# Performance work log

Hardware: AMD Instinct MI355X
Metric: run time of the kernel (lower is better)

Reference implementation:

```python
import jax, jax.numpy as jnp
import numpy as np

B, P, G, C = 16, 32768, 32, 81   # batch, priors, gt boxes per image, classes
IOU_THRESH = 0.5                 # matching() is IoU-threshold matching (standard SSD)
HMR = 3                          # hard_mining_ratio
BETA = 1.0                       # SmoothL1 beta


def _make_boxes(key, lead_shape):
    k1, k2 = jax.random.split(key)
    xy = jax.random.uniform(k1, lead_shape + (2,)) * 0.8
    wh = jax.random.uniform(k2, lead_shape + (2,)) * 0.2 + 0.05
    return jnp.concatenate([xy, xy + wh], axis=-1)  # valid x1y1x2y2 in [0,1]


def setup_inputs() -> dict:
    key = jax.random.key(0)
    ks = jax.random.split(key, 5)
    pred_boxes = _make_boxes(ks[0], (B, P))
    gt_boxes = _make_boxes(ks[1], (B, G))
    # guarantee matches exist: first G priors track the gt boxes closely
    noise = jax.random.normal(ks[2], (B, G, 4)) * 0.005
    pred_boxes = pred_boxes.at[:, :G, :].set(gt_boxes + noise)
    pred_confidences = jax.random.normal(ks[3], (B, P, C), dtype=jnp.float32)
    gt_labels = jax.random.randint(ks[4], (B, G), 0, C, dtype=jnp.int32)
    return {"pred_boxes": pred_boxes, "pred_confidences": pred_confidences,
            "gt_boxes": gt_boxes, "gt_labels": gt_labels}


def _iou(a, b):
    # a: [P,4], b: [G,4] in x1y1x2y2 -> [P,G]
    lt = jnp.maximum(a[:, None, :2], b[None, :, :2])
    rb = jnp.minimum(a[:, None, 2:], b[None, :, 2:])
    inter = jnp.prod(jnp.clip(rb - lt, 0.0), axis=-1)
    area_a = jnp.prod(jnp.clip(a[:, 2:] - a[:, :2], 0.0), axis=-1)
    area_b = jnp.prod(jnp.clip(b[:, 2:] - b[:, :2], 0.0), axis=-1)
    union = area_a[:, None] + area_b[None, :] - inter
    return inter / jnp.maximum(union, 1e-9)


def _smooth_l1(pred, gt):
    d = pred - gt
    ad = jnp.abs(d)
    return jnp.where(ad < BETA, 0.5 * d * d / BETA, ad - 0.5 * BETA)


def _per_image(boxes, conf, gboxes, glabels):
    # boxes [P,4], conf [P,C], gboxes [G,4], glabels [G]
    matches = _iou(boxes, gboxes) > IOU_THRESH          # [P,G]
    total = matches.sum()
    logsm = jax.nn.log_softmax(conf, axis=-1)            # [P,C]
    gathered = logsm[:, glabels]                         # [P,G] log p(label_g | prior_i)
    matches_loss = jnp.sum(jnp.where(matches, gathered, 0.0))
    # mean over the 4 coords, summed over matched (prior, gt) pairs
    sl1 = _smooth_l1(boxes[:, None, :], gboxes[None, :, :]).mean(axis=-1)  # [P,G]
    loc_loss = jnp.sum(jnp.where(matches, sl1, 0.0))
    # hard-negative mining over unmatched priors
    row_matched = matches.any(axis=1)                    # [P]
    sm_max = jnp.max(jax.nn.softmax(conf, axis=-1), axis=-1)  # [P], all > 0
    neg = jnp.where(row_matched, -1.0, sm_max)           # matched rows sort last
    neg = jnp.concatenate([neg, jnp.zeros((1,), neg.dtype)])  # source's extra slot (contributes log1p(0)=0)
    sorted_neg = -jnp.sort(-neg)                         # descending
    k = HMR * total
    keep = (jnp.arange(sorted_neg.shape[0]) < k) & (sorted_neg >= 0.0)
    nomatch_loss = jnp.sum(jnp.where(keep, jnp.log1p(sorted_neg), 0.0))
    return matches_loss, nomatch_loss, loc_loss, total


def reference(pred_boxes, pred_confidences, gt_boxes, gt_labels):
    m, n, l, t = jax.vmap(_per_image)(pred_boxes, pred_confidences, gt_boxes, gt_labels)
    conf_loss = -m.sum() + n.sum()
    # faithful to source: final division uses the LAST image's total_matches
    total_last = t[-1].astype(conf_loss.dtype)
    return (conf_loss + l.sum()) / total_last
```

## Files before the change

### kernel.cpp

```cpp
#include <hip/hip_runtime.h>
#include <hip/hip_bf16.h>
#include <math.h>

#define BB 16
#define PP 32768
#define GG 32
#define NC 81
#define BINSHIFT 13
#define NBINS 8192
#define LOWMASK 0x1FFFu
#define BINBASE 0x3B800000u
#define CAND_CAP 2048
#define SENT 0x7FFFFFFFu
#define SM_BLOCKS 2048
#define BLK_PER_IMG 128
#define NEGINF (-3.0e38f)

struct Accs {
  float m[BB]; float l[BB]; float n[BB];
  unsigned tot[BB]; unsigned rowm[BB];
  unsigned tbin[BB]; unsigned rem[BB]; unsigned candcnt[BB];
};

__device__ __forceinline__ int bin_of(unsigned bits) {
  int bin = ((int)bits - (int)BINBASE) >> BINSHIFT;
  return bin < 0 ? 0 : (bin > NBINS - 1 ? NBINS - 1 : bin);
}

__global__ void init_kernel(Accs* __restrict__ acc) {
  const int t = threadIdx.x;
  if (t < BB) {
    acc->m[t] = 0.f; acc->l[t] = 0.f; acc->n[t] = 0.f;
    acc->tot[t] = 0u; acc->rowm[t] = 0u; acc->candcnt[t] = 0u;
  }
}

__global__ __launch_bounds__(256) void main_kernel(
    const float* __restrict__ pred_boxes,
    const float* __restrict__ conf,
    const float* __restrict__ gt_boxes,
    const int*   __restrict__ gt_labels,
    float* __restrict__ neg,
    Accs* __restrict__ acc)
{
  const int tid  = threadIdx.x;
  const int j    = tid & 7;
  const int rsub = tid >> 3;
  const int b    = blockIdx.x / BLK_PER_IMG;
  const int loc  = blockIdx.x % BLK_PER_IMG;
  const int lane = tid & 63;
  const int w    = tid >> 6;

  __shared__ unsigned s_gm[NC + 3];
  __shared__ float pg[4], pl[4];
  __shared__ unsigned pc[4], pr[4];

  if (tid < NC + 3) s_gm[tid] = 0u;
  __syncthreads();
  if (tid < GG) atomicOr(&s_gm[gt_labels[b * GG + tid]], 1u << tid);
  __syncthreads();

  const float4* gtb = ((const float4*)gt_boxes) + b * GG;
  const float4 gA = gtb[j];
  const float4 gB = gtb[j + 8];
  const float4 gC = gtb[j + 16];
  const float4 gD = gtb[j + 24];
  const float abA = fmaxf(gA.z - gA.x, 0.f) * fmaxf(gA.w - gA.y, 0.f);
  const float abB = fmaxf(gB.z - gB.x, 0.f) * fmaxf(gB.w - gB.y, 0.f);
  const float abC = fmaxf(gC.z - gC.x, 0.f) * fmaxf(gC.w - gC.y, 0.f);
  const float abD = fmaxf(gD.z - gD.x, 0.f) * fmaxf(gD.w - gD.y, 0.f);

  const int  h  = rsub & 3;
  const bool j0 = (j == 0), j4 = (j == 4);
  const bool has3 = (j < 5);
  const float mA0 = (j0 && h > 0) ? NEGINF : 0.f;
  const float mA1 = (j0 && h > 1) ? NEGINF : 0.f;
  const float mA2 = (j0 && h > 2) ? NEGINF : 0.f;
  const float mC1 = (j4 && h < 1) ? NEGINF : 0.f;
  const float mC2 = (j4 && h < 2) ? NEGINF : 0.f;
  const float mC3 = (j4 && h < 3) ? NEGINF : 0.f;
  const int dA = 4 * j - h;
  const int dB = 4 * (j + 8) - h;
  const int dC = 4 * (j + 16) - h;

  const float4* cf = (const float4*)conf;
  const float4* pbf = (const float4*)pred_boxes;

  float t_g = 0.f, t_l = 0.f;
  unsigned t_c = 0u, t_r = 0u;

  int row = b * PP + loc * 32 + rsub;
  {
    const unsigned abase = (81u * (unsigned)row) >> 2;
  }
  unsigned abase0 = (81u * (unsigned)row) >> 2;
  float4 va = cf[abase0 + j];
  float4 vb = cf[abase0 + j + 8];
  float4 vc = has3 ? cf[abase0 + j + 16] : va;
  float4 pb = pbf[row];

  #pragma unroll
  for (int k = 0; k < 8; ++k) {
    float4 nva = va, nvb = vb, nvc = vc, npb = pb;
    if (k < 7) {
      const int nrow = row + BLK_PER_IMG * 32;
      const unsigned nab = (81u * (unsigned)nrow) >> 2;
      nva = cf[nab + j];
      nvb = cf[nab + j + 8];
      if (has3) nvc = cf[nab + j + 16]; else nvc = nva;
      npb = pbf[nrow];
    }

    const float a0 = va.x + mA0, a1 = va.y + mA1, a2 = va.z + mA2, a3 = va.w;
    float mx = fmaxf(fmaxf(a0, a1), fmaxf(a2, a3));
    float s  = __expf(a0) + __expf(a1) + __expf(a2) + __expf(a3);
    mx = fmaxf(mx, fmaxf(fmaxf(vb.x, vb.y), fmaxf(vb.z, vb.w)));
    s += __expf(vb.x) + __expf(vb.y) + __expf(vb.z) + __expf(vb.w);
    if (has3) {
      const float e0 = vc.x, e1 = vc.y + mC1, e2 = vc.z + mC2, e3 = vc.w + mC3;
      mx = fmaxf(mx, fmaxf(fmaxf(e0, e1), fmaxf(e2, e3)));
      s += __expf(e0) + __expf(e1) + __expf(e2) + __expf(e3);
    }
    mx = fmaxf(mx, __shfl_xor(mx, 1));  s += __shfl_xor(s, 1);
    mx = fmaxf(mx, __shfl_xor(mx, 2));  s += __shfl_xor(s, 2);
    mx = fmaxf(mx, __shfl_xor(mx, 4));  s += __shfl_xor(s, 4);
    const float lse = __logf(s);
    const float smx = __expf(mx - lse);

    const float aa = fmaxf(pb.z - pb.x, 0.f) * fmaxf(pb.w - pb.y, 0.f);
    unsigned msk = 0u;
    unsigned mymt = 0u;
    #define IOU_ONE(gb, ab, sh, bit)                                        \
    {                                                                       \
      const float ltx = fmaxf(pb.x, gb.x), lty = fmaxf(pb.y, gb.y);         \
      const float rbx = fminf(pb.z, gb.z), rby = fminf(pb.w, gb.w);         \
      const float inter = fmaxf(rbx - ltx, 0.f) * fmaxf(rby - lty, 0.f);    \
      const float uni = aa + ab - inter;                                    \
      const bool mt = inter > 0.5f * fmaxf(uni, 1e-9f);                     \
      msk  |= mt ? (1u << (j + sh)) : 0u;                                   \
      mymt |= mt ? (1u << bit) : 0u;                                        \
    }
    IOU_ONE(gA, abA, 0, 0)
    IOU_ONE(gB, abB, 8, 1)
    IOU_ONE(gC, abC, 16, 2)
    IOU_ONE(gD, abD, 24, 3)
    #undef IOU_ONE

    msk |= __shfl_xor(msk, 1); msk |= __shfl_xor(msk, 2); msk |= __shfl_xor(msk, 4);

    if (j == 0) neg[row] = (msk != 0u) ? -1.0f : smx;

    if (__any(msk != 0u)) {
      float lsum = 0.f;
      #define SL1_ONE(gb, bit)                                              \
      if (mymt & (1u << bit)) {                                             \
        const float d0 = pb.x - gb.x, d1 = pb.y - gb.y;                     \
        const float d2 = pb.z - gb.z, d3 = pb.w - gb.w;                     \
        float sl = 0.f, ad;                                                 \
        ad = fabsf(d0); sl += (ad < 1.f) ? 0.5f * d0 * d0 : ad - 0.5f;      \
        ad = fabsf(d1); sl += (ad < 1.f) ? 0.5f * d1 * d1 : ad - 0.5f;      \
        ad = fabsf(d2); sl += (ad < 1.f) ? 0.5f * d2 * d2 : ad - 0.5f;      \
        ad = fabsf(d3); sl += (ad < 1.f) ? 0.5f * d3 * d3 : ad - 0.5f;      \
        lsum += sl * 0.25f;                                                 \
      }
      SL1_ONE(gA, 0)
      SL1_ONE(gB, 1)
      SL1_ONE(gC, 2)
      SL1_ONE(gD, 3)
      #undef SL1_ONE
      t_l += lsum;

      if (msk != 0u) {
        float gsum = 0.f;
        if (dA >= 0) gsum += va.x * (float)__popc(msk & s_gm[dA]);
        if (dA + 1 >= 0) gsum += va.y * (float)__popc(msk & s_gm[dA + 1]);
        if (dA + 2 >= 0) gsum += va.z * (float)__popc(msk & s_gm[dA + 2]);
        gsum += va.w * (float)__popc(msk & s_gm[dA + 3]);
        gsum += vb.x * (float)__popc(msk & s_gm[dB]);
        gsum += vb.y * (float)__popc(msk & s_gm[dB + 1]);
        gsum += vb.z * (float)__popc(msk & s_gm[dB + 2]);
        gsum += vb.w * (float)__popc(msk & s_gm[dB + 3]);
        if (has3) {
          gsum += vc.x * (float)__popc(msk & s_gm[dC]);
          if (dC + 1 < NC) gsum += vc.y * (float)__popc(msk & s_gm[dC + 1]);
          if (dC + 2 < NC) gsum += vc.z * (float)__popc(msk & s_gm[dC + 2]);
          if (dC + 3 < NC) gsum += vc.w * (float)__popc(msk & s_gm[dC + 3]);
        }
        t_g += gsum;
        if (j == 0) {
          const unsigned cnt = (unsigned)__popc(msk);
          t_g -= (float)cnt * lse;
          t_c += cnt;
          t_r += 1u;
        }
      }
    }

    va = nva; vb = nvb; vc = nvc; pb = npb;
    row += BLK_PER_IMG * 32;
  }

  t_g += __shfl_xor(t_g, 1);  t_l += __shfl_xor(t_l, 1);  t_c += __shfl_xor(t_c, 1);  t_r += __shfl_xor(t_r, 1);
  t_g += __shfl_xor(t_g, 2);  t_l += __shfl_xor(t_l, 2);  t_c += __shfl_xor(t_c, 2);  t_r += __shfl_xor(t_r, 2);
  t_g += __shfl_xor(t_g, 4);  t_l += __shfl_xor(t_l, 4);  t_c += __shfl_xor(t_c, 4);  t_r += __shfl_xor(t_r, 4);
  t_g += __shfl_xor(t_g, 8);  t_l += __shfl_xor(t_l, 8);  t_c += __shfl_xor(t_c, 8);  t_r += __shfl_xor(t_r, 8);
  t_g += __shfl_xor(t_g, 16); t_l += __shfl_xor(t_l, 16); t_c += __shfl_xor(t_c, 16); t_r += __shfl_xor(t_r, 16);
  t_g += __shfl_xor(t_g, 32); t_l += __shfl_xor(t_l, 32); t_c += __shfl_xor(t_c, 32); t_r += __shfl_xor(t_r, 32);
  if (lane == 0) { pg[w] = t_g; pl[w] = t_l; pc[w] = t_c; pr[w] = t_r; }
  __syncthreads();
  if (tid == 0) {
    const unsigned c2 = pc[0] + pc[1] + pc[2] + pc[3];
    if (c2 > 0u) {
      atomicAdd(&acc->m[b],    pg[0] + pg[1] + pg[2] + pg[3]);
      atomicAdd(&acc->l[b],    pl[0] + pl[1] + pl[2] + pl[3]);
      atomicAdd(&acc->tot[b],  c2);
      atomicAdd(&acc->rowm[b], pr[0] + pr[1] + pr[2] + pr[3]);
    }
  }
}

__global__ __launch_bounds__(256) void thresh_kernel(const float* __restrict__ neg,
                                                     Accs* __restrict__ acc) {
  const int b = blockIdx.x, tid = threadIdx.x;
  __shared__ unsigned hist[NBINS];
  __shared__ unsigned ps[256];
  __shared__ unsigned s_ch, s_cb;

  const unsigned total  = acc->tot[b];
  const unsigned nvalid = PP - acc->rowm[b];
  unsigned K = 3u * total;
  if (K > nvalid) K = nvalid;
  if (K == 0u) {
    if (tid == 0) { acc->tbin[b] = SENT; acc->rem[b] = 0u; }
    return;
  }

  for (int i = tid; i < NBINS; i += 256) hist[i] = 0u;
  __syncthreads();

  const float4* nb = (const float4*)(neg + ((size_t)b << 15));
  for (int i = tid; i < PP / 4; i += 256) {
    const float4 v4 = nb[i];
    const float vv[4] = {v4.x, v4.y, v4.z, v4.w};
    #pragma unroll
    for (int q = 0; q < 4; ++q)
      if (vv[q] >= 0.f) atomicAdd(&hist[bin_of(__float_as_uint(vv[q]))], 1u);
  }
  __syncthreads();

  unsigned loc = 0;
  #pragma unroll
  for (int q = 0; q < NBINS / 256; ++q) loc += hist[tid * (NBINS / 256) + q];
  ps[tid] = loc;
  __syncthreads();
  for (int off = 1; off < 256; off <<= 1) {
    const unsigned v = (tid + off < 256) ? ps[tid + off] : 0u;
    __syncthreads();
    ps[tid] += v;
    __syncthreads();
  }
  {
    const unsigned above = (tid < 255) ? ps[tid + 1] : 0u;
    if (ps[tid] >= K && above < K) { s_ch = (unsigned)tid; s_cb = above; }
  }
  __syncthreads();
  const unsigned ch = s_ch, cb = s_cb;
  const int CH = NBINS / 256;
  if (tid < CH) ps[tid] = hist[ch * CH + tid];
  __syncthreads();
  for (int off = 1; off < CH; off <<= 1) {
    const unsigned v = (tid < CH && tid + off < CH) ? ps[tid + off] : 0u;
    __syncthreads();
    if (tid < CH) ps[tid] += v;
    __syncthreads();
  }
  if (tid < CH) {
    const unsigned above = cb + ((tid < CH - 1) ? ps[tid + 1] : 0u);
    if (above < K && cb + ps[tid] >= K) {
      acc->tbin[b] = ch * (unsigned)CH + (unsigned)tid;
      acc->rem[b]  = K - above;
    }
  }
}

__global__ __launch_bounds__(256) void sum_kernel(const float* __restrict__ neg,
                                                  float* __restrict__ cand,
                                                  Accs* __restrict__ acc) {
  const int b  = blockIdx.x >> 4;
  const int sl = blockIdx.x & 15;
  const unsigned t = acc->tbin[b];
  const float4* nb = (const float4*)(neg + ((size_t)b << 15)) + sl * 512;
  float sum = 0.f;
  #pragma unroll
  for (int it = 0; it < 2; ++it) {
    const float4 v4 = nb[threadIdx.x + it * 256];
    const float vv[4] = {v4.x, v4.y, v4.z, v4.w};
    #pragma unroll
    for (int q = 0; q < 4; ++q) {
      const float v = vv[q];
      if (v >= 0.f) {
        const unsigned bin = (unsigned)bin_of(__float_as_uint(v));
        if (bin > t) {
          sum += log1pf(v);
        } else if (bin == t) {
          const unsigned idx = atomicAdd(&acc->candcnt[b], 1u);
          if (idx < CAND_CAP) cand[(size_t)b * CAND_CAP + idx] = v;
        }
      }
    }
  }
  sum += __shfl_xor(sum, 1);  sum += __shfl_xor(sum, 2);  sum += __shfl_xor(sum, 4);
  sum += __shfl_xor(sum, 8);  sum += __shfl_xor(sum, 16); sum += __shfl_xor(sum, 32);
  if ((threadIdx.x & 63) == 0 && sum != 0.f) atomicAdd(&acc->n[b], sum);
}

__global__ __launch_bounds__(256) void refine_kernel(const float* __restrict__ neg,
                                                     const float* __restrict__ cand,
                                                     Accs* __restrict__ acc) {
  const int b = blockIdx.x, tid = threadIdx.x;
  __shared__ unsigned h2[NBINS];
  __shared__ unsigned ps[256];
  __shared__ unsigned s_thr, s_rem2;
  const unsigned t = acc->tbin[b];
  if (t == SENT) return;
  const unsigned rem = acc->rem[b];
  const unsigned cc  = acc->candcnt[b];
  const bool fb = (cc > CAND_CAP);
  const int n_src = fb ? PP : (int)cc;
  const float* src = fb ? (neg + ((size_t)b << 15)) : (cand + (size_t)b * CAND_CAP);

  for (int i = tid; i < NBINS; i += 256) h2[i] = 0u;
  __syncthreads();
  for (int i = tid; i < n_src; i += 256) {
    const float v = src[i];
    if (fb) {
      if (!(v >= 0.f) || (unsigned)bin_of(__float_as_uint(v)) != t) continue;
    }
    atomicAdd(&h2[__float_as_uint(v) & LOWMASK], 1u);
  }
  __syncthreads();

  unsigned loc = 0;
  #pragma unroll
  for (int q = 0; q < NBINS / 256; ++q) loc += h2[tid * (NBINS / 256) + q];
  ps[tid] = loc;
  __syncthreads();
  for (int off = 1; off < 256; off <<= 1) {
    const unsigned v = (tid + off < 256) ? ps[tid + off] : 0u;
    __syncthreads();
    ps[tid] += v;
    __syncthreads();
  }
  {
    const unsigned above = (tid < 255) ? ps[tid + 1] : 0u;
    if (ps[tid] >= rem && above < rem) {
      unsigned c = above;
      const int CH = NBINS / 256;
      for (int q = CH - 1; q >= 0; --q) {
        const unsigned hb = h2[tid * CH + q];
        if (c + hb >= rem) { s_thr = (unsigned)(tid * CH + q); s_rem2 = rem - c; break; }
        c += hb;
      }
    }
  }
  __syncthreads();
  const unsigned thr = s_thr, rem2 = s_rem2;

  float sum = 0.f;
  for (int i = tid; i < n_src; i += 256) {
    const float v = src[i];
    if (fb) {
      if (!(v >= 0.f) || (unsigned)bin_of(__float_as_uint(v)) != t) continue;
    }
    if ((__float_as_uint(v) & LOWMASK) > thr) sum += log1pf(v);
  }
  sum += __shfl_xor(sum, 1);  sum += __shfl_xor(sum, 2);  sum += __shfl_xor(sum, 4);
  sum += __shfl_xor(sum, 8);  sum += __shfl_xor(sum, 16); sum += __shfl_xor(sum, 32);
  if ((tid & 63) == 0 && sum != 0.f) atomicAdd(&acc->n[b], sum);
  if (tid == 0 && rem2 > 0u) {
    const unsigned tb = BINBASE + (t << BINSHIFT) + thr;
    atomicAdd(&acc->n[b], (float)rem2 * log1pf(__uint_as_float(tb)));
  }
}

__global__ void finish_kernel(const Accs* __restrict__ acc, float* __restrict__ out) {
  if (threadIdx.x == 0) {
    float conf = 0.f, loc = 0.f;
    #pragma unroll
    for (int b = 0; b < BB; ++b) {
      conf += -acc->m[b] + acc->n[b];
      loc  += acc->l[b];
    }
    out[0] = (conf + loc) / (float)acc->tot[BB - 1];
  }
}

extern "C" void kernel_launch(void* const* d_in, const int* in_sizes, int n_in,
                              void* d_out, int out_size, void* d_ws, size_t ws_size,
                              hipStream_t stream) {
  const float* pred_boxes = (const float*)d_in[0];
  const float* conf       = (const float*)d_in[1];
  const float* gt_boxes   = (const float*)d_in[2];
  const int*   gt_labels  = (const int*)d_in[3];
  float* out = (float*)d_out;

  char* ws = (char*)d_ws;
  float* neg  = (float*)ws;
  float* cand = (float*)(ws + (size_t)BB * PP * 4);
  Accs*  acc  = (Accs*)(ws + (size_t)BB * PP * 4 + (size_t)BB * CAND_CAP * 4);

  hipLaunchKernelGGL(init_kernel, dim3(1), dim3(64), 0, stream, acc);
  hipLaunchKernelGGL(main_kernel, dim3(SM_BLOCKS), dim3(256), 0, stream,
                     pred_boxes, conf, gt_boxes, gt_labels, neg, acc);
  hipLaunchKernelGGL(thresh_kernel, dim3(BB), dim3(256), 0, stream, neg, acc);
  hipLaunchKernelGGL(sum_kernel, dim3(BB * 16), dim3(256), 0, stream, neg, cand, acc);
  hipLaunchKernelGGL(refine_kernel, dim3(BB), dim3(256), 0, stream, neg, cand, acc);
  hipLaunchKernelGGL(finish_kernel, dim3(1), dim3(64), 0, stream, acc, out);
}
```

Before: 104.5 us.

## Fuse threshold, sum and refine kernels into single per-image select kernel

```diff
diff --git a/kernel.cpp b/kernel.cpp
--- a/kernel.cpp
+++ b/kernel.cpp
@@ -10,8 +10,6 @@
 #define NBINS 8192
 #define LOWMASK 0x1FFFu
 #define BINBASE 0x3B800000u
-#define CAND_CAP 2048
-#define SENT 0x7FFFFFFFu
 #define SM_BLOCKS 2048
 #define BLK_PER_IMG 128
 #define NEGINF (-3.0e38f)
@@ -19,7 +17,6 @@
 struct Accs {
   float m[BB]; float l[BB]; float n[BB];
   unsigned tot[BB]; unsigned rowm[BB];
-  unsigned tbin[BB]; unsigned rem[BB]; unsigned candcnt[BB];
 };
 
 __device__ __forceinline__ int bin_of(unsigned bits) {
@@ -31,7 +28,7 @@
   const int t = threadIdx.x;
   if (t < BB) {
     acc->m[t] = 0.f; acc->l[t] = 0.f; acc->n[t] = 0.f;
-    acc->tot[t] = 0u; acc->rowm[t] = 0u; acc->candcnt[t] = 0u;
+    acc->tot[t] = 0u; acc->rowm[t] = 0u;
   }
 }
 
@@ -83,20 +80,17 @@
   const int dB = 4 * (j + 8) - h;
   const int dC = 4 * (j + 16) - h;
 
-  const float4* cf = (const float4*)conf;
+  const float4* cf  = (const float4*)conf;
   const float4* pbf = (const float4*)pred_boxes;
 
   float t_g = 0.f, t_l = 0.f;
   unsigned t_c = 0u, t_r = 0u;
 
   int row = b * PP + loc * 32 + rsub;
-  {
-    const unsigned abase = (81u * (unsigned)row) >> 2;
-  }
-  unsigned abase0 = (81u * (unsigned)row) >> 2;
-  float4 va = cf[abase0 + j];
-  float4 vb = cf[abase0 + j + 8];
-  float4 vc = has3 ? cf[abase0 + j + 16] : va;
+  const unsigned ab0 = (81u * (unsigned)row) >> 2;
+  float4 va = cf[ab0 + j];
+  float4 vb = cf[ab0 + j + 8];
+  float4 vc = has3 ? cf[ab0 + j + 16] : va;
   float4 pb = pbf[row];
 
   #pragma unroll
@@ -219,23 +213,26 @@
   }
 }
 
-__global__ __launch_bounds__(256) void thresh_kernel(const float* __restrict__ neg,
-                                                     Accs* __restrict__ acc) {
+__global__ __launch_bounds__(256) void select_kernel(const float* __restrict__ neg,
+                                                     Accs* __restrict__ acc)
+{
   const int b = blockIdx.x, tid = threadIdx.x;
   __shared__ unsigned hist[NBINS];
+  __shared__ unsigned h2[NBINS];
   __shared__ unsigned ps[256];
-  __shared__ unsigned s_ch, s_cb;
+  __shared__ unsigned s_ch, s_cb, s_t, s_remv, s_thr, s_rem2;
+  __shared__ float spart[4];
 
   const unsigned total  = acc->tot[b];
   const unsigned nvalid = PP - acc->rowm[b];
   unsigned K = 3u * total;
   if (K > nvalid) K = nvalid;
   if (K == 0u) {
-    if (tid == 0) { acc->tbin[b] = SENT; acc->rem[b] = 0u; }
+    if (tid == 0) acc->n[b] = 0.f;
     return;
   }
 
-  for (int i = tid; i < NBINS; i += 256) hist[i] = 0u;
+  for (int i = tid; i < NBINS; i += 256) { hist[i] = 0u; h2[i] = 0u; }
   __syncthreads();
 
   const float4* nb = (const float4*)(neg + ((size_t)b << 15));
@@ -248,139 +245,97 @@
   }
   __syncthreads();
 
-  unsigned loc = 0;
-  #pragma unroll
-  for (int q = 0; q < NBINS / 256; ++q) loc += hist[tid * (NBINS / 256) + q];
-  ps[tid] = loc;
-  __syncthreads();
-  for (int off = 1; off < 256; off <<= 1) {
-    const unsigned v = (tid + off < 256) ? ps[tid + off] : 0u;
-    __syncthreads();
-    ps[tid] += v;
-    __syncthreads();
-  }
   {
+    unsigned loc = 0;
+    #pragma unroll
+    for (int q = 0; q < 32; ++q) loc += hist[tid * 32 + q];
+    ps[tid] = loc;
+    __syncthreads();
+    for (int off = 1; off < 256; off <<= 1) {
+      const unsigned v = (tid + off < 256) ? ps[tid + off] : 0u;
+      __syncthreads();
+      ps[tid] += v;
+      __syncthreads();
+    }
     const unsigned above = (tid < 255) ? ps[tid + 1] : 0u;
     if (ps[tid] >= K && above < K) { s_ch = (unsigned)tid; s_cb = above; }
-  }
-  __syncthreads();
-  const unsigned ch = s_ch, cb = s_cb;
-  const int CH = NBINS / 256;
-  if (tid < CH) ps[tid] = hist[ch * CH + tid];
-  __syncthreads();
-  for (int off = 1; off < CH; off <<= 1) {
-    const unsigned v = (tid < CH && tid + off < CH) ? ps[tid + off] : 0u;
-    __syncthreads();
-    if (tid < CH) ps[tid] += v;
-    __syncthreads();
-  }
-  if (tid < CH) {
-    const unsigned above = cb + ((tid < CH - 1) ? ps[tid + 1] : 0u);
-    if (above < K && cb + ps[tid] >= K) {
-      acc->tbin[b] = ch * (unsigned)CH + (unsigned)tid;
-      acc->rem[b]  = K - above;
-    }
-  }
-}
-
-__global__ __launch_bounds__(256) void sum_kernel(const float* __restrict__ neg,
-                                                  float* __restrict__ cand,
-                                                  Accs* __restrict__ acc) {
-  const int b  = blockIdx.x >> 4;
-  const int sl = blockIdx.x & 15;
-  const unsigned t = acc->tbin[b];
-  const float4* nb = (const float4*)(neg + ((size_t)b << 15)) + sl * 512;
+    __syncthreads();
+    const unsigned ch = s_ch, cb = s_cb;
+    if (tid < 32) ps[tid] = hist[ch * 32 + tid];
+    __syncthreads();
+    for (int off = 1; off < 32; off <<= 1) {
+      const unsigned v = (tid < 32 && tid + off < 32) ? ps[tid + off] : 0u;
+      __syncthreads();
+      if (tid < 32) ps[tid] += v;
+      __syncthreads();
+    }
+    if (tid < 32) {
+      const unsigned ab2 = cb + ((tid < 31) ? ps[tid + 1] : 0u);
+      if (ab2 < K && cb + ps[tid] >= K) { s_t = ch * 32u + (unsigned)tid; s_remv = K - ab2; }
+    }
+    __syncthreads();
+  }
+  const unsigned t   = s_t;
+  const unsigned rem = s_remv;
+
   float sum = 0.f;
-  #pragma unroll
-  for (int it = 0; it < 2; ++it) {
-    const float4 v4 = nb[threadIdx.x + it * 256];
+  for (int i = tid; i < PP / 4; i += 256) {
+    const float4 v4 = nb[i];
     const float vv[4] = {v4.x, v4.y, v4.z, v4.w};
     #pragma unroll
     for (int q = 0; q < 4; ++q) {
       const float v = vv[q];
       if (v >= 0.f) {
-        const unsigned bin = (unsigned)bin_of(__float_as_uint(v));
-        if (bin > t) {
-          sum += log1pf(v);
-        } else if (bin == t) {
-          const unsigned idx = atomicAdd(&acc->candcnt[b], 1u);
-          if (idx < CAND_CAP) cand[(size_t)b * CAND_CAP + idx] = v;
-        }
+        const unsigned bits = __float_as_uint(v);
+        const unsigned bin = (unsigned)bin_of(bits);
+        if (bin > t) sum += log1pf(v);
+        else if (bin == t) atomicAdd(&h2[bits & LOWMASK], 1u);
       }
     }
   }
-  sum += __shfl_xor(sum, 1);  sum += __shfl_xor(sum, 2);  sum += __shfl_xor(sum, 4);
-  sum += __shfl_xor(sum, 8);  sum += __shfl_xor(sum, 16); sum += __shfl_xor(sum, 32);
-  if ((threadIdx.x & 63) == 0 && sum != 0.f) atomicAdd(&acc->n[b], sum);
-}
-
-__global__ __launch_bounds__(256) void refine_kernel(const float* __restrict__ neg,
-                                                     const float* __restrict__ cand,
-                                                     Accs* __restrict__ acc) {
-  const int b = blockIdx.x, tid = threadIdx.x;
-  __shared__ unsigned h2[NBINS];
-  __shared__ unsigned ps[256];
-  __shared__ unsigned s_thr, s_rem2;
-  const unsigned t = acc->tbin[b];
-  if (t == SENT) return;
-  const unsigned rem = acc->rem[b];
-  const unsigned cc  = acc->candcnt[b];
-  const bool fb = (cc > CAND_CAP);
-  const int n_src = fb ? PP : (int)cc;
-  const float* src = fb ? (neg + ((size_t)b << 15)) : (cand + (size_t)b * CAND_CAP);
-
-  for (int i = tid; i < NBINS; i += 256) h2[i] = 0u;
-  __syncthreads();
-  for (int i = tid; i < n_src; i += 256) {
-    const float v = src[i];
-    if (fb) {
-      if (!(v >= 0.f) || (unsigned)bin_of(__float_as_uint(v)) != t) continue;
-    }
-    atomicAdd(&h2[__float_as_uint(v) & LOWMASK], 1u);
-  }
-  __syncthreads();
-
-  unsigned loc = 0;
-  #pragma unroll
-  for (int q = 0; q < NBINS / 256; ++q) loc += h2[tid * (NBINS / 256) + q];
-  ps[tid] = loc;
-  __syncthreads();
-  for (int off = 1; off < 256; off <<= 1) {
-    const unsigned v = (tid + off < 256) ? ps[tid + off] : 0u;
-    __syncthreads();
-    ps[tid] += v;
-    __syncthreads();
-  }
+  __syncthreads();
+
   {
+    unsigned loc = 0;
+    #pragma unroll
+    for (int q = 0; q < 32; ++q) loc += h2[tid * 32 + q];
+    ps[tid] = loc;
+    __syncthreads();
+    for (int off = 1; off < 256; off <<= 1) {
+      const unsigned v = (tid + off < 256) ? ps[tid + off] : 0u;
+      __syncthreads();
+      ps[tid] += v;
+      __syncthreads();
+    }
     const unsigned above = (tid < 255) ? ps[tid + 1] : 0u;
     if (ps[tid] >= rem && above < rem) {
       unsigned c = above;
-      const int CH = NBINS / 256;
-      for (int q = CH - 1; q >= 0; --q) {
-        const unsigned hb = h2[tid * CH + q];
-        if (c + hb >= rem) { s_thr = (unsigned)(tid * CH + q); s_rem2 = rem - c; break; }
+      for (int q = 31; q >= 0; --q) {
+        const unsigned hb = h2[tid * 32 + q];
+        if (c + hb >= rem) { s_thr = (unsigned)(tid * 32 + q); s_rem2 = rem - c; break; }
         c += hb;
       }
     }
-  }
-  __syncthreads();
+    __syncthreads();
+  }
   const unsigned thr = s_thr, rem2 = s_rem2;
 
-  float sum = 0.f;
-  for (int i = tid; i < n_src; i += 256) {
-    const float v = src[i];
-    if (fb) {
-      if (!(v >= 0.f) || (unsigned)bin_of(__float_as_uint(v)) != t) continue;
-    }
-    if ((__float_as_uint(v) & LOWMASK) > thr) sum += log1pf(v);
-  }
+  const unsigned base_t = BINBASE + (t << BINSHIFT);
+  #pragma unroll
+  for (int q = 0; q < 32; ++q) {
+    const unsigned low = (unsigned)tid * 32u + (unsigned)q;
+    const unsigned c = h2[low];
+    if (low > thr && c > 0u)
+      sum += (float)c * log1pf(__uint_as_float(base_t + low));
+  }
+  if (tid == 0)
+    sum += (float)rem2 * log1pf(__uint_as_float(base_t + thr));
+
   sum += __shfl_xor(sum, 1);  sum += __shfl_xor(sum, 2);  sum += __shfl_xor(sum, 4);
   sum += __shfl_xor(sum, 8);  sum += __shfl_xor(sum, 16); sum += __shfl_xor(sum, 32);
-  if ((tid & 63) == 0 && sum != 0.f) atomicAdd(&acc->n[b], sum);
-  if (tid == 0 && rem2 > 0u) {
-    const unsigned tb = BINBASE + (t << BINSHIFT) + thr;
-    atomicAdd(&acc->n[b], (float)rem2 * log1pf(__uint_as_float(tb)));
-  }
+  if ((tid & 63) == 0) spart[tid >> 6] = sum;
+  __syncthreads();
+  if (tid == 0) acc->n[b] = spart[0] + spart[1] + spart[2] + spart[3];
 }
 
 __global__ void finish_kernel(const Accs* __restrict__ acc, float* __restrict__ out) {
@@ -405,15 +360,12 @@
   float* out = (float*)d_out;
 
   char* ws = (char*)d_ws;
-  float* neg  = (float*)ws;
-  float* cand = (float*)(ws + (size_t)BB * PP * 4);
-  Accs*  acc  = (Accs*)(ws + (size_t)BB * PP * 4 + (size_t)BB * CAND_CAP * 4);
+  float* neg = (float*)ws;
+  Accs*  acc = (Accs*)(ws + (size_t)BB * PP * 4);
 
   hipLaunchKernelGGL(init_kernel, dim3(1), dim3(64), 0, stream, acc);
   hipLaunchKernelGGL(main_kernel, dim3(SM_BLOCKS), dim3(256), 0, stream,
                      pred_boxes, conf, gt_boxes, gt_labels, neg, acc);
-  hipLaunchKernelGGL(thresh_kernel, dim3(BB), dim3(256), 0, stream, neg, acc);
-  hipLaunchKernelGGL(sum_kernel, dim3(BB * 16), dim3(256), 0, stream, neg, cand, acc);
-  hipLaunchKernelGGL(refine_kernel, dim3(BB), dim3(256), 0, stream, neg, cand, acc);
+  hipLaunchKernelGGL(select_kernel, dim3(BB), dim3(256), 0, stream, neg, acc);
   hipLaunchKernelGGL(finish_kernel, dim3(1), dim3(64), 0, stream, acc, out);
 }
```

Result: slower. 126.8 us (+21.4%).
